# Kernel optimization log

Measured on AMD Instinct MI355X. Metric: run time of the kernel, lower is better.

Reference implementation:

```python
import jax, jax.numpy as jnp
import numpy as np

HEADS = 16

def setup_inputs() -> dict:
    key = jax.random.key(0)
    ks = jax.random.split(key, 5)
    B, T, D = 4, 2048, 1024
    scale = 0.02
    return {
        "x": jax.random.normal(ks[0], (B, T, D), dtype=jnp.float32),
        "W_attn": jax.random.normal(ks[1], (D, 3 * D), dtype=jnp.float32) * scale,
        "b_attn": jax.random.normal(ks[2], (3 * D,), dtype=jnp.float32) * scale,
        "W_proj": jax.random.normal(ks[3], (D, D), dtype=jnp.float32) * scale,
        "b_proj": jax.random.normal(ks[4], (D,), dtype=jnp.float32) * scale,
    }

def reference(x, W_attn, b_attn, W_proj, b_proj):
    B, T, D = x.shape
    H = HEADS
    hd = D // H
    qkv = x @ W_attn + b_attn                      # [B, T, 3D]
    q, k, v = jnp.split(qkv, 3, axis=2)
    # [B, T, H, hd] -> [B, H, T, hd]
    q = q.reshape(B, T, H, hd).transpose(0, 2, 1, 3)
    k = k.reshape(B, T, H, hd).transpose(0, 2, 1, 3)
    v = v.reshape(B, T, H, hd).transpose(0, 2, 1, 3)
    scale = hd ** 0.5
    scores = jnp.einsum("bhqd,bhkd->bhqk", q, k) / scale
    causal = jnp.tril(jnp.ones((T, T), dtype=bool))
    scores = jnp.where(causal, scores, -jnp.inf)
    attn = jax.nn.softmax(scores, axis=-1)
    out = jnp.einsum("bhqk,bhkd->bhqd", attn, v)    # [B, H, T, hd]
    out = out.transpose(0, 2, 1, 3).reshape(B, T, D)
    return out @ W_proj + b_proj
```

## Files before the change

kernel.cpp:

```cpp
#include <hip/hip_runtime.h>
#include <hip/hip_bf16.h>

using bf16 = __hip_bfloat16;
typedef __attribute__((ext_vector_type(8))) __bf16 bf16x8;
typedef __attribute__((ext_vector_type(4))) short s16x4;
typedef __attribute__((ext_vector_type(4))) float f32x4;

#define B_   4
#define T_   2048
#define D_   1024
#define H_   16
#define HD_  64
#define BH_  (B_ * H_)
#define BT_  (B_ * T_)

#define QSCALE 0.18033688011112042f

__device__ __forceinline__ void gld_lds16(const void* g, void* l) {
    __builtin_amdgcn_global_load_lds(
        (const __attribute__((address_space(1))) unsigned int*)g,
        (__attribute__((address_space(3))) unsigned int*)l,
        16, 0, 0);
}

__device__ __forceinline__ f32x4 mfma16(s16x4 a, s16x4 b, f32x4 c) {
#if defined(__HIP_DEVICE_COMPILE__)
  #if __has_builtin(__builtin_amdgcn_mfma_f32_16x16x16bf16_1k)
    return __builtin_amdgcn_mfma_f32_16x16x16bf16_1k(a, b, c, 0, 0, 0);
  #else
    f32x4 d;
    asm volatile("v_mfma_f32_16x16x16_bf16 %0, %1, %2, %3\n\ts_nop 7\n\ts_nop 7"
                 : "=v"(d) : "v"(a), "v"(b), "v"(c));
    return d;
  #endif
#else
    (void)a; (void)b;
    return c;
#endif
}

__device__ __forceinline__ unsigned bfbits(float x) {
    return (unsigned)__builtin_bit_cast(unsigned short, __float2bfloat16(x));
}

__global__ void cast_kernel(const float* __restrict__ in, bf16* __restrict__ out, int n4) {
    int i = blockIdx.x * 256 + threadIdx.x;
    if (i >= n4) return;
    float4 v = reinterpret_cast<const float4*>(in)[i];
    union { bf16 h[4]; uint2 u; } tmp;
    tmp.h[0] = __float2bfloat16(v.x);
    tmp.h[1] = __float2bfloat16(v.y);
    tmp.h[2] = __float2bfloat16(v.z);
    tmp.h[3] = __float2bfloat16(v.w);
    reinterpret_cast<uint2*>(out)[i] = tmp.u;
}

__global__ void transpose_cast(const float* __restrict__ W, bf16* __restrict__ Wt,
                               int K, int N) {
    __shared__ float tile[32][33];
    int nb = blockIdx.x * 32, kb = blockIdx.y * 32;
    int tx = threadIdx.x, ty = threadIdx.y;
    #pragma unroll
    for (int i = 0; i < 32; i += 8)
        tile[ty + i][tx] = W[(size_t)(kb + ty + i) * N + nb + tx];
    __syncthreads();
    #pragma unroll
    for (int i = 0; i < 32; i += 8)
        Wt[(size_t)(nb + ty + i) * K + kb + tx] = __float2bfloat16(tile[tx][ty + i]);
}

template <int MODE>
__global__ __launch_bounds__(256)
void gemm_bt(const bf16* __restrict__ A, const bf16* __restrict__ Bt,
             const float* __restrict__ bias,
             bf16* __restrict__ Qo, bf16* __restrict__ Ko, bf16* __restrict__ Vo,
             float* __restrict__ Fo, int K) {
    const int bm = blockIdx.x * 128;
    const int bn = blockIdx.y * 128;
    const int tid  = threadIdx.x;
    const int wid  = tid >> 6;
    const int lane = tid & 63;
    const int wr = (wid >> 1) * 64;
    const int wc = (wid & 1) * 64;
    const int ln_g = lane >> 4;
    const int ln_c = lane & 15;

    __shared__ bf16 sm[2][2][128][32];

    f32x4 acc[4][4] = {};

    const int g_row0 = wid * 32 + (lane >> 2);
    const int g_chk  = ((lane & 3) ^ ((lane >> 3) & 3)) * 8;
    const int l_row0 = wid * 32;
    const int colx = (ln_g * 16) ^ (((ln_c >> 1) & 3) << 4);

#define STAGE(BUF_, K0_) {                                                              \
    gld_lds16(&A [(size_t)(bm + g_row0)      * K + (K0_) + g_chk], &sm[BUF_][0][l_row0][0]);      \
    gld_lds16(&A [(size_t)(bm + g_row0 + 16) * K + (K0_) + g_chk], &sm[BUF_][0][l_row0 + 16][0]); \
    gld_lds16(&Bt[(size_t)(bn + g_row0)      * K + (K0_) + g_chk], &sm[BUF_][1][l_row0][0]);      \
    gld_lds16(&Bt[(size_t)(bn + g_row0 + 16) * K + (K0_) + g_chk], &sm[BUF_][1][l_row0 + 16][0]); }

#define COMPUTE(BUF_) {                                                                  \
    bf16x8 af[4], bfr[4];                                                                \
    _Pragma("unroll")                                                                    \
    for (int m = 0; m < 4; ++m)                                                          \
        af[m] = *reinterpret_cast<const bf16x8*>(                                        \
            (const char*)&sm[BUF_][0][wr + m * 16 + ln_c][0] + colx);                    \
    _Pragma("unroll")                                                                    \
    for (int n = 0; n < 4; ++n)                                                          \
        bfr[n] = *reinterpret_cast<const bf16x8*>(                                       \
            (const char*)&sm[BUF_][1][wc + n * 16 + ln_c][0] + colx);                    \
    _Pragma("unroll")                                                                    \
    for (int m = 0; m < 4; ++m)                                                          \
        _Pragma("unroll")                                                                \
        for (int n = 0; n < 4; ++n)                                                      \
            acc[m][n] = __builtin_amdgcn_mfma_f32_16x16x32_bf16(af[m], bfr[n],           \
                                                                 acc[m][n], 0, 0, 0); }

    const int NT = K >> 5;
    STAGE(0, 0);
    __syncthreads();

    for (int t = 0; t < NT - 2; t += 2) {
        STAGE(1, (t + 1) * 32);
        COMPUTE(0);
        __syncthreads();
        STAGE(0, (t + 2) * 32);
        COMPUTE(1);
        __syncthreads();
    }
    STAGE(1, (NT - 1) * 32);
    COMPUTE(0);
    __syncthreads();
    COMPUTE(1);

#undef STAGE
#undef COMPUTE

    #pragma unroll
    for (int m = 0; m < 4; ++m) {
        #pragma unroll
        for (int n = 0; n < 4; ++n) {
            const int col = bn + wc + n * 16 + ln_c;
            const float bcol = bias[col];
            #pragma unroll
            for (int j = 0; j < 4; ++j) {
                const int row = bm + wr + m * 16 + ln_g * 4 + j;
                float v = acc[m][n][j] + bcol;
                if (MODE == 0) {
                    const int part = col >> 10;
                    const int cc = col & 1023;
                    const int h = cc >> 6, d = cc & 63;
                    const int b = row >> 11, t = row & 2047;
                    const int bh = b * H_ + h;
                    if (part == 0)
                        Qo[((size_t)bh * T_ + t) * HD_ + d] = __float2bfloat16(v * QSCALE);
                    else if (part == 1)
                        Ko[((size_t)bh * T_ + t) * HD_ + d] = __float2bfloat16(v);
                    else
                        Vo[((size_t)bh * HD_ + d) * T_ + t] = __float2bfloat16(v);
                } else {
                    Fo[(size_t)row * D_ + col] = v;
                }
            }
        }
    }
}

__global__ __launch_bounds__(256, 4)
void attn_kernel(const bf16* __restrict__ Q, const bf16* __restrict__ K,
                 const bf16* __restrict__ Vt, bf16* __restrict__ ctx) {
    const int bh = blockIdx.x & 63;
    const int qt = 31 - (blockIdx.x >> 6);
    const int tid  = threadIdx.x;
    const int wave = tid >> 6;
    const int lane = tid & 63;
    const int ln_g = lane >> 4;
    const int ln_c = lane & 15;

    const bf16* Qp = Q  + (size_t)bh * T_ * HD_;
    const bf16* Kp = K  + (size_t)bh * T_ * HD_;
    const bf16* Vp = Vt + (size_t)bh * HD_ * T_;

    __shared__ bf16 Ks[64][72];
    __shared__ bf16 Vs[64][72];

    const int srow = tid >> 3;
    const int sc8  = (tid & 7) * 8;

    const int b = bh >> 4, h = bh & 15;

    const int qbase = qt * 64;
    const int qglob = qbase + wave * 16 + ln_c;

    const bf16x8 qf0 = *reinterpret_cast<const bf16x8*>(&Qp[(size_t)qglob * HD_ + ln_g * 8]);
    const bf16x8 qf1 = *reinterpret_cast<const bf16x8*>(&Qp[(size_t)qglob * HD_ + 32 + ln_g * 8]);

    f32x4 o[4] = {};
    float m = -INFINITY, l = 0.f;

    const int nk = qt + 1;

    int4 kr0, kr1, vr0, vr1;
    kr0 = *reinterpret_cast<const int4*>(&Kp[(size_t)srow * HD_ + sc8]);
    kr1 = *reinterpret_cast<const int4*>(&Kp[(size_t)(srow + 32) * HD_ + sc8]);
    vr0 = *reinterpret_cast<const int4*>(&Vp[(size_t)srow * T_ + sc8]);
    vr1 = *reinterpret_cast<const int4*>(&Vp[(size_t)(srow + 32) * T_ + sc8]);
    *reinterpret_cast<int4*>(&Ks[srow][sc8])      = kr0;
    *reinterpret_cast<int4*>(&Ks[srow + 32][sc8]) = kr1;
    *reinterpret_cast<int4*>(&Vs[srow][sc8])      = vr0;
    *reinterpret_cast<int4*>(&Vs[srow + 32][sc8]) = vr1;
    __syncthreads();

    for (int it = 0; it < nk; ++it) {
        const int kb = it * 64;
        const bool notlast = (it + 1 < nk);
        if (notlast) {
            const int kn = kb + 64;
            kr0 = *reinterpret_cast<const int4*>(&Kp[(size_t)(kn + srow) * HD_ + sc8]);
            kr1 = *reinterpret_cast<const int4*>(&Kp[(size_t)(kn + srow + 32) * HD_ + sc8]);
            vr0 = *reinterpret_cast<const int4*>(&Vp[(size_t)srow * T_ + kn + sc8]);
            vr1 = *reinterpret_cast<const int4*>(&Vp[(size_t)(srow + 32) * T_ + kn + sc8]);
        }

        f32x4 st[4];
        __builtin_amdgcn_s_setprio(1);
        #pragma unroll
        for (int kk = 0; kk < 4; ++kk) {
            bf16x8 kfa = *reinterpret_cast<const bf16x8*>(&Ks[kk * 16 + ln_c][ln_g * 8]);
            bf16x8 kfb = *reinterpret_cast<const bf16x8*>(&Ks[kk * 16 + ln_c][32 + ln_g * 8]);
            f32x4 z = {0.f, 0.f, 0.f, 0.f};
            z = __builtin_amdgcn_mfma_f32_16x16x32_bf16(kfa, qf0, z, 0, 0, 0);
            z = __builtin_amdgcn_mfma_f32_16x16x32_bf16(kfb, qf1, z, 0, 0, 0);
            st[kk] = z;
        }
        __builtin_amdgcn_s_setprio(0);

        if (!notlast) {
            #pragma unroll
            for (int kk = 0; kk < 4; ++kk)
                #pragma unroll
                for (int j = 0; j < 4; ++j)
                    if (kb + kk * 16 + ln_g * 4 + j > qglob) st[kk][j] = -INFINITY;
        }

        float mx = -INFINITY;
        #pragma unroll
        for (int kk = 0; kk < 4; ++kk)
            #pragma unroll
            for (int j = 0; j < 4; ++j)
                mx = fmaxf(mx, st[kk][j]);
        if (!__all(mx - m <= 8.f)) {
            float r = fmaxf(mx, __shfl_xor(mx, 16));
            r = fmaxf(r, __shfl_xor(r, 32));
            const float mnew = fmaxf(m, r);
            const float alpha = exp2f(m - mnew);
            l *= alpha;
            #pragma unroll
            for (int dt = 0; dt < 4; ++dt)
                #pragma unroll
                for (int j = 0; j < 4; ++j)
                    o[dt][j] *= alpha;
            m = mnew;
        }

        #pragma unroll
        for (int kk = 0; kk < 4; ++kk) {
            float p0 = exp2f(st[kk][0] - m);
            float p1 = exp2f(st[kk][1] - m);
            float p2 = exp2f(st[kk][2] - m);
            float p3 = exp2f(st[kk][3] - m);
            l += (p0 + p1) + (p2 + p3);
            uint2 pw;
            pw.x = bfbits(p0) | (bfbits(p1) << 16);
            pw.y = bfbits(p2) | (bfbits(p3) << 16);
            const s16x4 ps = __builtin_bit_cast(s16x4, pw);
            __builtin_amdgcn_s_setprio(1);
            #pragma unroll
            for (int dt = 0; dt < 4; ++dt) {
                s16x4 vf = *reinterpret_cast<const s16x4*>(
                    &Vs[dt * 16 + ln_c][kk * 16 + ln_g * 4]);
                o[dt] = mfma16(vf, ps, o[dt]);
            }
            __builtin_amdgcn_s_setprio(0);
        }

        if (notlast) {
            __syncthreads();
            *reinterpret_cast<int4*>(&Ks[srow][sc8])      = kr0;
            *reinterpret_cast<int4*>(&Ks[srow + 32][sc8]) = kr1;
            *reinterpret_cast<int4*>(&Vs[srow][sc8])      = vr0;
            *reinterpret_cast<int4*>(&Vs[srow + 32][sc8]) = vr1;
            __syncthreads();
        }
    }

    l += __shfl_xor(l, 16);
    l += __shfl_xor(l, 32);
    const float inv = 1.0f / l;
    bf16* dst = ctx + ((size_t)(b * T_ + qglob)) * D_ + h * HD_;
    #pragma unroll
    for (int dt = 0; dt < 4; ++dt) {
        union { bf16 hh[4]; uint2 u; } ok;
        #pragma unroll
        for (int j = 0; j < 4; ++j)
            ok.hh[j] = __float2bfloat16(o[dt][j] * inv);
        *reinterpret_cast<uint2*>(&dst[dt * 16 + ln_g * 4]) = ok.u;
    }
}

extern "C" void kernel_launch(void* const* d_in, const int* in_sizes, int n_in,
                              void* d_out, int out_size, void* d_ws, size_t ws_size,
                              hipStream_t stream) {
    const float* x      = (const float*)d_in[0];
    const float* W_attn = (const float*)d_in[1];
    const float* b_attn = (const float*)d_in[2];
    const float* W_proj = (const float*)d_in[3];
    const float* b_proj = (const float*)d_in[4];
    float* out = (float*)d_out;

    char* ws = (char*)d_ws;
    bf16* xh  = (bf16*)ws;  ws += (size_t)BT_ * D_ * 2;
    bf16* WaT = (bf16*)ws;  ws += (size_t)3 * D_ * D_ * 2;
    bf16* WpT = (bf16*)ws;  ws += (size_t)D_ * D_ * 2;
    bf16* Qb  = (bf16*)ws;  ws += (size_t)BH_ * T_ * HD_ * 2;
    bf16* Kb  = (bf16*)ws;  ws += (size_t)BH_ * T_ * HD_ * 2;
    bf16* Vb  = (bf16*)ws;  ws += (size_t)BH_ * T_ * HD_ * 2;
    bf16* ctx = (bf16*)ws;  ws += (size_t)BT_ * D_ * 2;

    cast_kernel<<<(BT_ * D_ / 4 + 255) / 256, 256, 0, stream>>>(x, xh, BT_ * D_ / 4);
    transpose_cast<<<dim3(3 * D_ / 32, D_ / 32), dim3(32, 8), 0, stream>>>(W_attn, WaT, D_, 3 * D_);
    transpose_cast<<<dim3(D_ / 32, D_ / 32), dim3(32, 8), 0, stream>>>(W_proj, WpT, D_, D_);

    gemm_bt<0><<<dim3(BT_ / 128, 3 * D_ / 128), 256, 0, stream>>>(
        xh, WaT, b_attn, Qb, Kb, Vb, nullptr, D_);

    attn_kernel<<<dim3(BH_ * 32), 256, 0, stream>>>(Qb, Kb, Vb, ctx);

    gemm_bt<1><<<dim3(BT_ / 128, D_ / 128), 256, 0, stream>>>(
        ctx, WpT, b_proj, nullptr, nullptr, nullptr, out, D_);
}
```

Baseline: 185.5 us.

## Triple-buffer GEMM LDS staging with partial vmcnt waits

Replaces the double-buffered LDS pipeline in the bf16 GEMM with three stages, so two K-tiles of loads are in flight while one is computed. The full __syncthreads drain is swapped for s_waitcnt vmcnt(4) plus a raw barrier, which waits only for the oldest stage. K becomes a compile-time constant so the loop count is fixed at 10 iterations of three tiles. This uses more LDS per block, which may reduce occupancy, and the hand-written waitcnt logic depends on the exact number of outstanding loads per stage.

```diff
diff --git a/kernel.cpp b/kernel.cpp
--- a/kernel.cpp
+++ b/kernel.cpp
@@ -74,7 +74,8 @@
 void gemm_bt(const bf16* __restrict__ A, const bf16* __restrict__ Bt,
              const float* __restrict__ bias,
              bf16* __restrict__ Qo, bf16* __restrict__ Ko, bf16* __restrict__ Vo,
-             float* __restrict__ Fo, int K) {
+             float* __restrict__ Fo) {
+    constexpr int K = 1024;
     const int bm = blockIdx.x * 128;
     const int bn = blockIdx.y * 128;
     const int tid  = threadIdx.x;
@@ -85,7 +86,7 @@
     const int ln_g = lane >> 4;
     const int ln_c = lane & 15;
 
-    __shared__ bf16 sm[2][2][128][32];
+    __shared__ bf16 sm[3][2][128][32];
 
     f32x4 acc[4][4] = {};
 
@@ -94,22 +95,22 @@
     const int l_row0 = wid * 32;
     const int colx = (ln_g * 16) ^ (((ln_c >> 1) & 3) << 4);
 
-#define STAGE(BUF_, K0_) {                                                              \
-    gld_lds16(&A [(size_t)(bm + g_row0)      * K + (K0_) + g_chk], &sm[BUF_][0][l_row0][0]);      \
-    gld_lds16(&A [(size_t)(bm + g_row0 + 16) * K + (K0_) + g_chk], &sm[BUF_][0][l_row0 + 16][0]); \
-    gld_lds16(&Bt[(size_t)(bn + g_row0)      * K + (K0_) + g_chk], &sm[BUF_][1][l_row0][0]);      \
-    gld_lds16(&Bt[(size_t)(bn + g_row0 + 16) * K + (K0_) + g_chk], &sm[BUF_][1][l_row0 + 16][0]); }
-
-#define COMPUTE(BUF_) {                                                                  \
+#define STAGE(S_, K0_) {                                                              \
+    gld_lds16(&A [(size_t)(bm + g_row0)      * K + (K0_) + g_chk], &sm[S_][0][l_row0][0]);      \
+    gld_lds16(&A [(size_t)(bm + g_row0 + 16) * K + (K0_) + g_chk], &sm[S_][0][l_row0 + 16][0]); \
+    gld_lds16(&Bt[(size_t)(bn + g_row0)      * K + (K0_) + g_chk], &sm[S_][1][l_row0][0]);      \
+    gld_lds16(&Bt[(size_t)(bn + g_row0 + 16) * K + (K0_) + g_chk], &sm[S_][1][l_row0 + 16][0]); }
+
+#define COMPUTE(S_) {                                                                    \
     bf16x8 af[4], bfr[4];                                                                \
     _Pragma("unroll")                                                                    \
     for (int m = 0; m < 4; ++m)                                                          \
         af[m] = *reinterpret_cast<const bf16x8*>(                                        \
-            (const char*)&sm[BUF_][0][wr + m * 16 + ln_c][0] + colx);                    \
+            (const char*)&sm[S_][0][wr + m * 16 + ln_c][0] + colx);                      \
     _Pragma("unroll")                                                                    \
     for (int n = 0; n < 4; ++n)                                                          \
         bfr[n] = *reinterpret_cast<const bf16x8*>(                                       \
-            (const char*)&sm[BUF_][1][wc + n * 16 + ln_c][0] + colx);                    \
+            (const char*)&sm[S_][1][wc + n * 16 + ln_c][0] + colx);                      \
     _Pragma("unroll")                                                                    \
     for (int m = 0; m < 4; ++m)                                                          \
         _Pragma("unroll")                                                                \
@@ -117,25 +118,30 @@
             acc[m][n] = __builtin_amdgcn_mfma_f32_16x16x32_bf16(af[m], bfr[n],           \
                                                                  acc[m][n], 0, 0, 0); }
 
-    const int NT = K >> 5;
+#define WAITV4 { asm volatile("s_waitcnt vmcnt(4) lgkmcnt(0)" ::: "memory");             \
+                 __builtin_amdgcn_s_barrier();                                           \
+                 __builtin_amdgcn_sched_barrier(0); }
+#define WAITV0 { asm volatile("s_waitcnt vmcnt(0) lgkmcnt(0)" ::: "memory");             \
+                 __builtin_amdgcn_s_barrier();                                           \
+                 __builtin_amdgcn_sched_barrier(0); }
+
     STAGE(0, 0);
-    __syncthreads();
-
-    for (int t = 0; t < NT - 2; t += 2) {
-        STAGE(1, (t + 1) * 32);
-        COMPUTE(0);
-        __syncthreads();
-        STAGE(0, (t + 2) * 32);
-        COMPUTE(1);
-        __syncthreads();
+    STAGE(1, 32);
+
+    #pragma unroll 1
+    for (int i = 0; i < 10; ++i) {
+        const int kb = i * 96;
+        WAITV4; STAGE(2, kb + 64);  COMPUTE(0);
+        WAITV4; STAGE(0, kb + 96);  COMPUTE(1);
+        WAITV4; STAGE(1, kb + 128); COMPUTE(2);
     }
-    STAGE(1, (NT - 1) * 32);
-    COMPUTE(0);
-    __syncthreads();
-    COMPUTE(1);
+    WAITV4; COMPUTE(0);
+    WAITV0; COMPUTE(1);
 
 #undef STAGE
 #undef COMPUTE
+#undef WAITV4
+#undef WAITV0
 
     #pragma unroll
     for (int m = 0; m < 4; ++m) {
@@ -333,10 +339,10 @@
     transpose_cast<<<dim3(D_ / 32, D_ / 32), dim3(32, 8), 0, stream>>>(W_proj, WpT, D_, D_);
 
     gemm_bt<0><<<dim3(BT_ / 128, 3 * D_ / 128), 256, 0, stream>>>(
-        xh, WaT, b_attn, Qb, Kb, Vb, nullptr, D_);
+        xh, WaT, b_attn, Qb, Kb, Vb, nullptr);
 
     attn_kernel<<<dim3(BH_ * 32), 256, 0, stream>>>(Qb, Kb, Vb, ctx);
 
     gemm_bt<1><<<dim3(BT_ / 128, D_ / 128), 256, 0, stream>>>(
-        ctx, WpT, b_proj, nullptr, nullptr, nullptr, out, D_);
-}
+        ctx, WpT, b_proj, nullptr, nullptr, nullptr, out);
+}
```

Result: no change. 186.2 us (+0.4%).
